# Performance work log

Hardware: AMD Instinct MI355X
Metric: run time of the kernel (lower is better)

Reference implementation:

```python
import jax, jax.numpy as jnp
import numpy as np

N = 65536   # total nodes
E = 1048576 # total edges (avg degree 16)
B = 512     # graphs in batch
H = 4       # gat1 heads
C = 64      # per-head channels / GNN_HIDDEN


def segment_softmax(logits, seg, num_segments):
    # numerically stable softmax over segments (PyG softmax semantics, eps=1e-16)
    m = jax.ops.segment_max(logits, seg, num_segments=num_segments)
    m = jnp.where(jnp.isfinite(m), m, 0.0)
    e = jnp.exp(logits - m[seg])
    s = jax.ops.segment_sum(e, seg, num_segments=num_segments)
    return e / (s[seg] + 1e-16)


def gat_conv(x, edge_index, edge_attr, W, att_src, att_dst, We, att_edge, bias, heads, out_ch, concat):
    # PyG GATConv with edge_dim, add_self_loops=False
    n = x.shape[0]
    h = (x @ W).reshape(n, heads, out_ch)                 # (N,H,C)
    src, dst = edge_index[0], edge_index[1]
    a_s = jnp.sum(h * att_src, axis=-1)                   # (N,H)
    a_d = jnp.sum(h * att_dst, axis=-1)                   # (N,H)
    he = (edge_attr @ We).reshape(-1, heads, out_ch)      # (E,H,C)
    a_e = jnp.sum(he * att_edge, axis=-1)                 # (E,H)
    alpha = jax.nn.leaky_relu(a_s[src] + a_d[dst] + a_e, negative_slope=0.2)
    alpha = segment_softmax(alpha, dst, n)                # softmax over incoming edges per dst
    out = jax.ops.segment_sum(h[src] * alpha[..., None], dst, num_segments=n)  # (N,H,C)
    out = out.reshape(n, heads * out_ch) if concat else out.mean(axis=1)
    return out + bias


def setup_inputs() -> dict:
    key = jax.random.key(0)
    ks = jax.random.split(key, 24)
    s = 0.05
    d = {}
    d["global_feat"] = jax.random.normal(ks[0], (B, 512), jnp.float32)
    d["x"] = jax.random.normal(ks[1], (N, 13), jnp.float32)
    d["roi_feats"] = jax.random.normal(ks[2], (N, 256), jnp.float32)
    d["edge_index"] = jax.random.randint(ks[3], (2, E), 0, N)
    d["edge_attr"] = jax.random.normal(ks[4], (E, 5), jnp.float32)
    d["batch_vec"] = jnp.sort(jax.random.randint(ks[5], (N,), 0, B))
    # roi_proj / scene_proj
    d["roi_W"] = jax.random.normal(ks[6], (256, 64), jnp.float32) * s
    d["roi_b"] = jnp.zeros((64,), jnp.float32)
    d["scene_W"] = jax.random.normal(ks[7], (512, 128), jnp.float32) * s
    d["scene_b"] = jnp.zeros((128,), jnp.float32)
    d["g1_W"] = jax.random.normal(ks[8], (77, H * C), jnp.float32) * s
    d["g1_att_src"] = jax.random.normal(ks[9], (H, C), jnp.float32) * s
    d["g1_att_dst"] = jax.random.normal(ks[10], (H, C), jnp.float32) * s
    d["g1_We"] = jax.random.normal(ks[11], (5, H * C), jnp.float32) * s
    d["g1_att_edge"] = jax.random.normal(ks[12], (H, C), jnp.float32) * s
    d["g1_bias"] = jnp.zeros((H * C,), jnp.float32)
    # gat2: 256 -> 64, 1 head
    d["g2_W"] = jax.random.normal(ks[13], (H * C, C), jnp.float32) * s
    d["g2_att_src"] = jax.random.normal(ks[14], (1, C), jnp.float32) * s
    d["g2_att_dst"] = jax.random.normal(ks[15], (1, C), jnp.float32) * s
    d["g2_We"] = jax.random.normal(ks[16], (5, C), jnp.float32) * s
    d["g2_att_edge"] = jax.random.normal(ks[17], (1, C), jnp.float32) * s
    d["g2_bias"] = jnp.zeros((C,), jnp.float32)
    # attention pooling gate + classifier
    d["gate_W"] = jax.random.normal(ks[18], (C, 1), jnp.float32) * s
    d["gate_b"] = jnp.zeros((1,), jnp.float32)
    d["cls1_W"] = jax.random.normal(ks[19], (128 + C, 64), jnp.float32) * s
    d["cls1_b"] = jnp.zeros((64,), jnp.float32)
    d["cls2_W"] = jax.random.normal(ks[20], (64, 3), jnp.float32) * s
    d["cls2_b"] = jnp.zeros((3,), jnp.float32)
    return d


def reference(global_feat, x, roi_feats, edge_index, edge_attr, batch_vec,
              roi_W, roi_b, scene_W, scene_b,
              g1_W, g1_att_src, g1_att_dst, g1_We, g1_att_edge, g1_bias,
              g2_W, g2_att_src, g2_att_dst, g2_We, g2_att_edge, g2_bias,
              gate_W, gate_b, cls1_W, cls1_b, cls2_W, cls2_b):
    scene = global_feat @ scene_W + scene_b                       # (B,128)
    vis = jax.nn.relu(roi_feats @ roi_W + roi_b)                  # (N,64)
    h = jnp.concatenate([x, vis], axis=-1)                        # (N,77)
    h = jax.nn.relu(gat_conv(h, edge_index, edge_attr, g1_W, g1_att_src, g1_att_dst, g1_We, g1_att_edge, g1_bias, H, C, True))
    h = gat_conv(h, edge_index, edge_attr, g2_W, g2_att_src, g2_att_dst, g2_We, g2_att_edge, g2_bias, 1, C, False)  # (N,64)
    # GlobalAttention pooling
    gate = segment_softmax((h @ gate_W + gate_b)[:, 0], batch_vec, B)
    rel = jax.ops.segment_sum(gate[:, None] * h, batch_vec, num_segments=B)  # (B,64)
    comb = jnp.concatenate([scene, rel], axis=-1)                 # (B,192)
    hid = jax.nn.relu(comb @ cls1_W + cls1_b)                     # dropout off (eval)
    return hid @ cls2_W + cls2_b                                  # (B,3)
```

## Files before the change

kernel.cpp:

```cpp
#include <hip/hip_runtime.h>

#define N_NODES 65536
#define N_EDGES 1048576
#define NB      512

typedef unsigned short u16;
typedef unsigned int   u32;
typedef unsigned long long u64;

typedef __attribute__((ext_vector_type(8))) short bf16x8;
typedef __attribute__((ext_vector_type(4))) float f32x4;

__device__ __forceinline__ float bf2f(u16 u) { return __uint_as_float(((u32)u) << 16); }
__device__ __forceinline__ float lo16(u32 u) { return __uint_as_float(u << 16); }
__device__ __forceinline__ float hi16(u32 u) { return __uint_as_float(u & 0xffff0000u); }
__device__ __forceinline__ u16 f2bf(float f) {
    u32 u = __float_as_uint(f);
    u32 r = (u + 0x7fffu + ((u >> 16) & 1u)) >> 16;
    return (u16)r;
}
__device__ __forceinline__ u32 pk2(float a, float b) {
    return (u32)f2bf(a) | ((u32)f2bf(b) << 16);
}
__device__ __forceinline__ float wsum(float v) {
    for (int o = 32; o; o >>= 1) v += __shfl_xor(v, o, 64);
    return v;
}
__device__ __forceinline__ float wmax(float v) {
    for (int o = 32; o; o >>= 1) v = fmaxf(v, __shfl_xor(v, o, 64));
    return v;
}

__global__ void k_prep(const float* g1We, const float* g1ae, const float* g2We, const float* g2ae,
                       float* M1, float* M2) {
    int t = threadIdx.x;
    if (t < 20) {
        int j = t >> 2, h = t & 3;
        float s = 0.f;
        for (int c = 0; c < 64; c++) s += g1We[j * 256 + h * 64 + c] * g1ae[h * 64 + c];
        M1[t] = s;
    } else if (t < 25) {
        int j = t - 20;
        float s = 0.f;
        for (int c = 0; c < 64; c++) s += g2We[j * 64 + c] * g2ae[c];
        M2[j] = s;
    }
}

__global__ void k_wt1(const float* __restrict__ g1W, u16* __restrict__ Wt) {
    int c = blockIdx.x;
    int k = threadIdx.x;
    float v = 0.f;
    if (k < 77) {
        int ko = (k < 64) ? (13 + k) : (k - 64);
        v = g1W[(size_t)ko * 256 + c];
    }
    Wt[(size_t)c * 96 + k] = f2bf(v);
}

__global__ void k_wtv(const float* __restrict__ roiW, u16* __restrict__ Wt) {
    int c = blockIdx.x;
    int k = threadIdx.x;
    Wt[(size_t)c * 256 + k] = f2bf(roiW[(size_t)k * 64 + c]);
}

__global__ __launch_bounds__(256) void k_scene(const float* __restrict__ gf, const float* __restrict__ W,
                                               const float* __restrict__ bias, float* __restrict__ scene) {
    int idx = blockIdx.x * 256 + threadIdx.x;
    int b = idx >> 7, j = idx & 127;
    float acc = 0.f;
    for (int k = 0; k < 512; k++) acc += gf[b * 512 + k] * W[k * 128 + j];
    scene[idx] = acc + bias[j];
}

__global__ __launch_bounds__(256) void k_hist(const int* ei, int* cnt) {
    int e = blockIdx.x * 256 + threadIdx.x;
    atomicAdd(&cnt[ei[N_EDGES + e]], 1);
}

__global__ __launch_bounds__(256) void k_scan_blk(const int* __restrict__ cnt, int* __restrict__ pre,
                                                  int* __restrict__ bsum) {
    __shared__ int sd[256];
    int t = threadIdx.x, b = blockIdx.x;
    int base = b * 1024 + t * 4;
    int4 c = *(const int4*)(cnt + base);
    int s = c.x + c.y + c.z + c.w;
    sd[t] = s;
    __syncthreads();
    for (int off = 1; off < 256; off <<= 1) {
        int v = (t >= off) ? sd[t - off] : 0;
        __syncthreads();
        sd[t] += v;
        __syncthreads();
    }
    int excl = sd[t] - s;
    int4 p;
    p.x = excl;
    p.y = excl + c.x;
    p.z = excl + c.x + c.y;
    p.w = excl + c.x + c.y + c.z;
    *(int4*)(pre + base) = p;
    if (t == 255) bsum[b] = sd[255];
}

__global__ __launch_bounds__(64) void k_scan_top(int* bsum) {
    int t = threadIdx.x;
    int v = bsum[t];
    int inc = v;
    for (int off = 1; off < 64; off <<= 1) {
        int u = __shfl_up(inc, off, 64);
        if (t >= off) inc += u;
    }
    bsum[t] = inc - v;
}

__global__ __launch_bounds__(256) void k_scan_fix(const int* __restrict__ pre, const int* __restrict__ bsum,
                                                  int* __restrict__ row_ptr, int* __restrict__ coarse_cur) {
    int i = blockIdx.x * 256 + threadIdx.x;
    int v = pre[i] + bsum[i >> 10];
    row_ptr[i] = v;
    if ((i & 255) == 0) coarse_cur[i >> 8] = v;
    if (i == 0) row_ptr[N_NODES] = N_EDGES;
}

__global__ __launch_bounds__(256) void k_bucket(const int* __restrict__ ei, int* coarse_cur,
                                                u32* __restrict__ bpack, int* __restrict__ bsrc) {
    __shared__ u32 stageP[4096];
    __shared__ int stageS[4096];
    __shared__ int bcnt[256], bscan[256], boff[256], gbase[256];
    int t = threadIdx.x;
    int e0 = blockIdx.x * 4096;
    bcnt[t] = 0;
    __syncthreads();
    int dreg[16], sreg[16];
    for (int it = 0; it < 16; it++) {
        int e = e0 + it * 256 + t;
        int dd = ei[N_EDGES + e];
        dreg[it] = dd;
        sreg[it] = ei[e];
        atomicAdd(&bcnt[dd >> 8], 1);
    }
    __syncthreads();
    int v = bcnt[t];
    bscan[t] = v;
    __syncthreads();
    for (int off = 1; off < 256; off <<= 1) {
        int u = (t >= off) ? bscan[t - off] : 0;
        __syncthreads();
        bscan[t] += u;
        __syncthreads();
    }
    boff[t] = bscan[t] - v;
    gbase[t] = v ? atomicAdd(&coarse_cur[t], v) : 0;
    __syncthreads();
    for (int it = 0; it < 16; it++) {
        int e = e0 + it * 256 + t;
        int b = dreg[it] >> 8;
        int pos = atomicAdd(&boff[b], 1);
        stageP[pos] = ((u32)e << 12) | (u32)(dreg[it] & 255);
        stageS[pos] = sreg[it];
    }
    __syncthreads();
    for (int idx = t; idx < 4096; idx += 256) {
        int lo = 0, hi = 255;
        while (lo < hi) { int mid = (lo + hi) >> 1; if (bscan[mid] > idx) hi = mid; else lo = mid + 1; }
        int b = lo;
        int g = gbase[b] + (idx - (bscan[b] - bcnt[b]));
        bpack[g] = stageP[idx];
        bsrc[g] = stageS[idx];
    }
}

__global__ __launch_bounds__(256) void k_sortb(const u32* __restrict__ bpack, const int* __restrict__ bsrc,
                                               const int* __restrict__ row_ptr,
                                               int* __restrict__ eord, int* __restrict__ ssrc) {
    __shared__ int cur[256];
    int t = threadIdx.x, b = blockIdx.x;
    int nbase = b * 256;
    cur[t] = row_ptr[nbase + t];
    __syncthreads();
    int beg = row_ptr[nbase];
    int end = row_ptr[nbase + 256];
    for (int i = beg + t; i < end; i += 256) {
        u32 wd = bpack[i];
        int src = bsrc[i];
        int d8 = wd & 255;
        int pos = atomicAdd(&cur[d8], 1);
        eord[pos] = (int)(wd >> 12);
        ssrc[pos] = src;
    }
}

__global__ __launch_bounds__(256) void k_payload(const int* __restrict__ eord, const float* __restrict__ ea,
                                                 const float* __restrict__ M1, const float* __restrict__ M2,
                                                 float* __restrict__ a1es, float* __restrict__ a2es) {
    int pos = blockIdx.x * 256 + threadIdx.x;
    int e = eord[pos];
    float v[5];
    for (int j = 0; j < 5; j++) v[j] = ea[(size_t)e * 5 + j];
    float4 o;
    o.x = v[0]*M1[0]  + v[1]*M1[4]  + v[2]*M1[8]  + v[3]*M1[12] + v[4]*M1[16];
    o.y = v[0]*M1[1]  + v[1]*M1[5]  + v[2]*M1[9]  + v[3]*M1[13] + v[4]*M1[17];
    o.z = v[0]*M1[2]  + v[1]*M1[6]  + v[2]*M1[10] + v[3]*M1[14] + v[4]*M1[18];
    o.w = v[0]*M1[3]  + v[1]*M1[7]  + v[2]*M1[11] + v[3]*M1[15] + v[4]*M1[19];
    *(float4*)(a1es + (size_t)pos * 4) = o;
    a2es[pos] = v[0]*M2[0] + v[1]*M2[1] + v[2]*M2[2] + v[3]*M2[3] + v[4]*M2[4];
}

__global__ __launch_bounds__(256) void k_vis(const float* __restrict__ roi, const u16* __restrict__ Wt,
                                             const float* __restrict__ bias, u16* __restrict__ out) {
    __shared__ u16 At[64][264];
    int t = threadIdx.x;
    int w = t >> 6, l = t & 63, lo = l & 15, hi = l >> 4;
    int n0 = blockIdx.x * 64;
    int r = t >> 2, sub = t & 3;
    const float* rp = roi + (size_t)(n0 + r) * 256 + sub * 4;
    #pragma unroll
    for (int q = 0; q < 16; q++) {
        float4 v = *(const float4*)(rp + q * 16);
        uint2 p;
        p.x = pk2(v.x, v.y);
        p.y = pk2(v.z, v.w);
        *(uint2*)&At[r][q * 16 + sub * 4] = p;
    }
    float bb[4][4];
    #pragma unroll
    for (int cb = 0; cb < 4; cb++)
        #pragma unroll
        for (int rg = 0; rg < 4; rg++) bb[cb][rg] = bias[cb * 16 + hi * 4 + rg];
    __syncthreads();
    f32x4 acc[4];
    #pragma unroll
    for (int cb = 0; cb < 4; cb++) acc[cb] = (f32x4){0.f, 0.f, 0.f, 0.f};
    #pragma unroll
    for (int ks = 0; ks < 8; ks++) {
        bf16x8 af = *(const bf16x8*)(&At[w * 16 + lo][ks * 32 + hi * 8]);
        #pragma unroll
        for (int cb = 0; cb < 4; cb++) {
            bf16x8 wf = *(const bf16x8*)(Wt + (size_t)(cb * 16 + lo) * 256 + ks * 32 + hi * 8);
            acc[cb] = __builtin_amdgcn_mfma_f32_16x16x32_bf16(wf, af, acc[cb], 0, 0, 0);
        }
    }
    int nrow = n0 + w * 16 + lo;
    #pragma unroll
    for (int cb = 0; cb < 4; cb++) {
        uint2 p;
        p.x = pk2(fmaxf(acc[cb][0] + bb[cb][0], 0.f), fmaxf(acc[cb][1] + bb[cb][1], 0.f));
        p.y = pk2(fmaxf(acc[cb][2] + bb[cb][2], 0.f), fmaxf(acc[cb][3] + bb[cb][3], 0.f));
        *(uint2*)(out + (size_t)nrow * 64 + cb * 16 + hi * 4) = p;
    }
}

__global__ __launch_bounds__(256) void k_h1(const float* __restrict__ x, const u16* __restrict__ vis,
                                            const u16* __restrict__ Wt,
                                            const float* __restrict__ as_, const float* __restrict__ ad_,
                                            u16* __restrict__ h1, float* __restrict__ a1s,
                                            float* __restrict__ a1d) {
    __shared__ u16 At[64][104];
    int t = threadIdx.x;
    int w = t >> 6, l = t & 63, lo = l & 15, hi = l >> 4;
    int n0 = blockIdx.x * 64;
    int r = t >> 2, sub = t & 3;
    {
        const uint4* vp = (const uint4*)(vis + (size_t)(n0 + r) * 64 + sub * 16);
        uint4 v0 = vp[0], v1 = vp[1];
        *(uint4*)&At[r][sub * 16] = v0;
        *(uint4*)&At[r][sub * 16 + 8] = v1;
        if (sub == 0) {
            const float* xp = x + (size_t)(n0 + r) * 13;
            #pragma unroll
            for (int j = 0; j < 13; j++) At[r][64 + j] = f2bf(xp[j]);
        } else if (sub == 1) {
            #pragma unroll
            for (int j = 77; j < 96; j++) At[r][j] = 0;
        }
    }
    bf16x8 wf[4][3];
    float asv[4][4], adv[4][4];
    #pragma unroll
    for (int cb = 0; cb < 4; cb++) {
        #pragma unroll
        for (int ks = 0; ks < 3; ks++)
            wf[cb][ks] = *(const bf16x8*)(Wt + (size_t)(w * 64 + cb * 16 + lo) * 96 + ks * 32 + hi * 8);
        #pragma unroll
        for (int rg = 0; rg < 4; rg++) {
            asv[cb][rg] = as_[w * 64 + cb * 16 + hi * 4 + rg];
            adv[cb][rg] = ad_[w * 64 + cb * 16 + hi * 4 + rg];
        }
    }
    __syncthreads();
    #pragma unroll
    for (int nb = 0; nb < 4; nb++) {
        f32x4 acc[4];
        #pragma unroll
        for (int cb = 0; cb < 4; cb++) acc[cb] = (f32x4){0.f, 0.f, 0.f, 0.f};
        #pragma unroll
        for (int ks = 0; ks < 3; ks++) {
            bf16x8 af = *(const bf16x8*)(&At[nb * 16 + lo][ks * 32 + hi * 8]);
            #pragma unroll
            for (int cb = 0; cb < 4; cb++)
                acc[cb] = __builtin_amdgcn_mfma_f32_16x16x32_bf16(wf[cb][ks], af, acc[cb], 0, 0, 0);
        }
        int nrow = n0 + nb * 16 + lo;
        float ps = 0.f, pd = 0.f;
        #pragma unroll
        for (int cb = 0; cb < 4; cb++) {
            uint2 p;
            p.x = pk2(acc[cb][0], acc[cb][1]);
            p.y = pk2(acc[cb][2], acc[cb][3]);
            *(uint2*)(h1 + (size_t)nrow * 256 + w * 64 + cb * 16 + hi * 4) = p;
            ps += acc[cb][0] * asv[cb][0] + acc[cb][1] * asv[cb][1]
                + acc[cb][2] * asv[cb][2] + acc[cb][3] * asv[cb][3];
            pd += acc[cb][0] * adv[cb][0] + acc[cb][1] * adv[cb][1]
                + acc[cb][2] * adv[cb][2] + acc[cb][3] * adv[cb][3];
        }
        ps += __shfl_xor(ps, 16, 64); ps += __shfl_xor(ps, 32, 64);
        pd += __shfl_xor(pd, 16, 64); pd += __shfl_xor(pd, 32, 64);
        if (hi == 0) {
            a1s[nrow * 4 + w] = ps;
            a1d[nrow * 4 + w] = pd;
        }
    }
}

__global__ __launch_bounds__(256) void k_h2(const u16* __restrict__ A, const float* __restrict__ W,
                                            const float* __restrict__ as_, const float* __restrict__ ad_,
                                            u16* __restrict__ out, float* __restrict__ a2s,
                                            float* __restrict__ a2d) {
    __shared__ float At[64][68];
    __shared__ float Wl[64][68];
    int t = threadIdx.x;
    int n0 = blockIdx.x * 64;
    int cg = t & 15, rg = t >> 4;
    int sr = t >> 2, scs = (t & 3) * 16;
    float acc[4][4];
    for (int i = 0; i < 4; i++) for (int j = 0; j < 4; j++) acc[i][j] = 0.f;
    for (int kc = 0; kc < 4; kc++) {
        __syncthreads();
        const u16* ap = A + (size_t)(n0 + sr) * 256 + kc * 64 + scs;
        uint4 u0 = *(const uint4*)ap;
        uint4 u1 = *(const uint4*)(ap + 8);
        At[scs + 0][sr] = lo16(u0.x);  At[scs + 1][sr] = hi16(u0.x);
        At[scs + 2][sr] = lo16(u0.y);  At[scs + 3][sr] = hi16(u0.y);
        At[scs + 4][sr] = lo16(u0.z);  At[scs + 5][sr] = hi16(u0.z);
        At[scs + 6][sr] = lo16(u0.w);  At[scs + 7][sr] = hi16(u0.w);
        At[scs + 8][sr] = lo16(u1.x);  At[scs + 9][sr] = hi16(u1.x);
        At[scs + 10][sr] = lo16(u1.y); At[scs + 11][sr] = hi16(u1.y);
        At[scs + 12][sr] = lo16(u1.z); At[scs + 13][sr] = hi16(u1.z);
        At[scs + 14][sr] = lo16(u1.w); At[scs + 15][sr] = hi16(u1.w);
        const float* wp = W + (size_t)(kc * 64 + sr) * 64 + scs;
        *(float4*)&Wl[sr][scs + 0]  = *(const float4*)wp;
        *(float4*)&Wl[sr][scs + 4]  = *(const float4*)(wp + 4);
        *(float4*)&Wl[sr][scs + 8]  = *(const float4*)(wp + 8);
        *(float4*)&Wl[sr][scs + 12] = *(const float4*)(wp + 12);
        __syncthreads();
        for (int k = 0; k < 64; k++) {
            float4 a4 = *(const float4*)&At[k][rg * 4];
            float4 w4 = *(const float4*)&Wl[k][cg * 4];
            acc[0][0] += a4.x * w4.x; acc[0][1] += a4.x * w4.y; acc[0][2] += a4.x * w4.z; acc[0][3] += a4.x * w4.w;
            acc[1][0] += a4.y * w4.x; acc[1][1] += a4.y * w4.y; acc[1][2] += a4.y * w4.z; acc[1][3] += a4.y * w4.w;
            acc[2][0] += a4.z * w4.x; acc[2][1] += a4.z * w4.y; acc[2][2] += a4.z * w4.z; acc[2][3] += a4.z * w4.w;
            acc[3][0] += a4.w * w4.x; acc[3][1] += a4.w * w4.y; acc[3][2] += a4.w * w4.z; acc[3][3] += a4.w * w4.w;
        }
    }
    u32* outu = (u32*)out;
    for (int i = 0; i < 4; i++) {
        uint2 pk;
        pk.x = (u32)f2bf(acc[i][0]) | ((u32)f2bf(acc[i][1]) << 16);
        pk.y = (u32)f2bf(acc[i][2]) | ((u32)f2bf(acc[i][3]) << 16);
        *(uint2*)(outu + (size_t)(n0 + rg * 4 + i) * 32 + cg * 2) = pk;
    }
    float4 as4 = *(const float4*)(as_ + cg * 4);
    float4 ad4 = *(const float4*)(ad_ + cg * 4);
    #pragma unroll
    for (int i = 0; i < 4; i++) {
        float ps = acc[i][0] * as4.x + acc[i][1] * as4.y + acc[i][2] * as4.z + acc[i][3] * as4.w;
        float pd = acc[i][0] * ad4.x + acc[i][1] * ad4.y + acc[i][2] * ad4.z + acc[i][3] * ad4.w;
        for (int o = 1; o < 16; o <<= 1) { ps += __shfl_xor(ps, o, 64); pd += __shfl_xor(pd, o, 64); }
        if (cg == 0) {
            a2s[n0 + rg * 4 + i] = ps;
            a2d[n0 + rg * 4 + i] = pd;
        }
    }
}

__global__ __launch_bounds__(256) void k_soft1(const int* __restrict__ row_ptr, const int* __restrict__ ssrc,
                                               const float* __restrict__ a1s, const float* __restrict__ a1d,
                                               const float* __restrict__ a1es, float* __restrict__ w1,
                                               float2* __restrict__ minv1) {
    int t = threadIdx.x;
    int wv = t >> 6, L = t & 63;
    int n = blockIdx.x * 4 + wv;
    int h = L >> 4, j = L & 15;
    int beg = row_ptr[n], deg = row_ptr[n + 1] - beg;
    if (deg == 0) return;
    float adn = a1d[n * 4 + h];
    float m = -3.0e38f, s = 0.f;
    for (int i = j; i < deg; i += 16) {
        int pos = beg + i;
        float l = a1s[ssrc[pos] * 4 + h] + adn + a1es[(size_t)pos * 4 + h];
        l = (l > 0.f) ? l : 0.2f * l;
        w1[(size_t)pos * 4 + h] = l;
        if (l > m) { s = s * __expf(m - l) + 1.f; m = l; }
        else       { s += __expf(l - m); }
    }
    for (int o = 1; o < 16; o <<= 1) {
        float mo = __shfl_xor(m, o, 64), so = __shfl_xor(s, o, 64);
        float M = fmaxf(m, mo);
        s = s * __expf(m - M) + so * __expf(mo - M);
        m = M;
    }
    if (j == 0) minv1[n * 4 + h] = make_float2(m, 1.f / (s + 1e-16f));
}

__global__ __launch_bounds__(256) void k_gath1(const int* __restrict__ row_ptr, const int* __restrict__ ssrc,
                                               const float* __restrict__ w1, const float2* __restrict__ minv1,
                                               const u16* __restrict__ h1,
                                               const float* __restrict__ bias, u16* __restrict__ out1) {
    int t = threadIdx.x;
    int wv = t >> 6, L = t & 63;
    int n = blockIdx.x * 4 + wv;
    int beg = row_ptr[n], deg = row_ptr[n + 1] - beg;
    int halfE = L >> 5;
    int L32 = L & 31;
    int hd = L32 >> 3;
    float2 mi = (deg > 0) ? minv1[n * 4 + hd] : make_float2(0.f, 0.f);
    float acc[8];
    #pragma unroll
    for (int j = 0; j < 8; j++) acc[j] = 0.f;
    int last = beg + deg - 1;
    for (int i = 0; i < deg; i += 8) {
        int iA = i + halfE, iB = i + 2 + halfE, iC = i + 4 + halfE, iD = i + 6 + halfE;
        bool vA = iA < deg, vB = iB < deg, vC = iC < deg, vD = iD < deg;
        int cA = vA ? beg + iA : last, cB = vB ? beg + iB : last;
        int cC = vC ? beg + iC : last, cD = vD ? beg + iD : last;
        int sA = ssrc[cA], sB = ssrc[cB], sC = ssrc[cC], sD = ssrc[cD];
        float lA = w1[(size_t)cA * 4 + hd];
        float lB = w1[(size_t)cB * 4 + hd];
        float lC = w1[(size_t)cC * 4 + hd];
        float lD = w1[(size_t)cD * 4 + hd];
        float wA = vA ? __expf(lA - mi.x) * mi.y : 0.f;
        float wB = vB ? __expf(lB - mi.x) * mi.y : 0.f;
        float wC = vC ? __expf(lC - mi.x) * mi.y : 0.f;
        float wD = vD ? __expf(lD - mi.x) * mi.y : 0.f;
        uint4 uA = *((const uint4*)(h1 + (size_t)sA * 256) + L32);
        uint4 uB = *((const uint4*)(h1 + (size_t)sB * 256) + L32);
        uint4 uC = *((const uint4*)(h1 + (size_t)sC * 256) + L32);
        uint4 uD = *((const uint4*)(h1 + (size_t)sD * 256) + L32);
        acc[0] += wA * lo16(uA.x) + wB * lo16(uB.x) + wC * lo16(uC.x) + wD * lo16(uD.x);
        acc[1] += wA * hi16(uA.x) + wB * hi16(uB.x) + wC * hi16(uC.x) + wD * hi16(uD.x);
        acc[2] += wA * lo16(uA.y) + wB * lo16(uB.y) + wC * lo16(uC.y) + wD * lo16(uD.y);
        acc[3] += wA * hi16(uA.y) + wB * hi16(uB.y) + wC * hi16(uC.y) + wD * hi16(uD.y);
        acc[4] += wA * lo16(uA.z) + wB * lo16(uB.z) + wC * lo16(uC.z) + wD * lo16(uD.z);
        acc[5] += wA * hi16(uA.z) + wB * hi16(uB.z) + wC * hi16(uC.z) + wD * hi16(uD.z);
        acc[6] += wA * lo16(uA.w) + wB * lo16(uB.w) + wC * lo16(uC.w) + wD * lo16(uD.w);
        acc[7] += wA * hi16(uA.w) + wB * hi16(uB.w) + wC * hi16(uC.w) + wD * hi16(uD.w);
    }
    #pragma unroll
    for (int j = 0; j < 8; j++) acc[j] += __shfl_xor(acc[j], 32, 64);
    if (halfE == 0) {
        float4 b0 = *(const float4*)(bias + 8 * L32);
        float4 b1 = *(const float4*)(bias + 8 * L32 + 4);
        uint4 pk;
        pk.x = (u32)f2bf(fmaxf(acc[0] + b0.x, 0.f)) | ((u32)f2bf(fmaxf(acc[1] + b0.y, 0.f)) << 16);
        pk.y = (u32)f2bf(fmaxf(acc[2] + b0.z, 0.f)) | ((u32)f2bf(fmaxf(acc[3] + b0.w, 0.f)) << 16);
        pk.z = (u32)f2bf(fmaxf(acc[4] + b1.x, 0.f)) | ((u32)f2bf(fmaxf(acc[5] + b1.y, 0.f)) << 16);
        pk.w = (u32)f2bf(fmaxf(acc[6] + b1.z, 0.f)) | ((u32)f2bf(fmaxf(acc[7] + b1.w, 0.f)) << 16);
        *((uint4*)(out1 + (size_t)n * 256) + L32) = pk;
    }
}

__global__ __launch_bounds__(256) void k_soft2(const int* __restrict__ row_ptr, const int* __restrict__ ssrc,
                                               const float* __restrict__ a2s, const float* __restrict__ a2d,
                                               const float* __restrict__ a2es, float* __restrict__ w2,
                                               float2* __restrict__ minv2) {
    int t = threadIdx.x;
    int wv = t >> 6, L = t & 63;
    int g = L >> 4, j = L & 15;
    int n = blockIdx.x * 16 + wv * 4 + g;
    int beg = row_ptr[n], deg = row_ptr[n + 1] - beg;
    if (deg == 0) return;
    float adn = a2d[n];
    float m = -3.0e38f, s = 0.f;
    for (int i = j; i < deg; i += 16) {
        int pos = beg + i;
        float l = a2s[ssrc[pos]] + adn + a2es[pos];
        l = (l > 0.f) ? l : 0.2f * l;
        w2[pos] = l;
        if (l > m) { s = s * __expf(m - l) + 1.f; m = l; }
        else       { s += __expf(l - m); }
    }
    for (int o = 1; o < 16; o <<= 1) {
        float mo = __shfl_xor(m, o, 64), so = __shfl_xor(s, o, 64);
        float M = fmaxf(m, mo);
        s = s * __expf(m - M) + so * __expf(mo - M);
        m = M;
    }
    if (j == 0) minv2[n] = make_float2(m, 1.f / (s + 1e-16f));
}

__global__ __launch_bounds__(256) void k_gath2(const int* __restrict__ row_ptr, const int* __restrict__ ssrc,
                                               const float* __restrict__ w2, const float2* __restrict__ minv2,
                                               const u16* __restrict__ h2b,
                                               const float* __restrict__ bias, float* __restrict__ hfin) {
    int t = threadIdx.x;
    int wv = t >> 6, L = t & 63;
    int n = blockIdx.x * 4 + wv;
    int beg = row_ptr[n], deg = row_ptr[n + 1] - beg;
    int halfE = L >> 5;
    int L32 = L & 31;
    float2 mi = (deg > 0) ? minv2[n] : make_float2(0.f, 0.f);
    float a0 = 0.f, a1v = 0.f;
    int last = beg + deg - 1;
    const u32* h2u = (const u32*)h2b;
    for (int i = 0; i < deg; i += 8) {
        int iA = i + halfE, iB = i + 2 + halfE, iC = i + 4 + halfE, iD = i + 6 + halfE;
        bool vA = iA < deg, vB = iB < deg, vC = iC < deg, vD = iD < deg;
        int cA = vA ? beg + iA : last, cB = vB ? beg + iB : last;
        int cC = vC ? beg + iC : last, cD = vD ? beg + iD : last;
        int sA = ssrc[cA], sB = ssrc[cB], sC = ssrc[cC], sD = ssrc[cD];
        float lA = w2[cA], lB = w2[cB], lC = w2[cC], lD = w2[cD];
        float wA = vA ? __expf(lA - mi.x) * mi.y : 0.f;
        float wB = vB ? __expf(lB - mi.x) * mi.y : 0.f;
        float wC = vC ? __expf(lC - mi.x) * mi.y : 0.f;
        float wD = vD ? __expf(lD - mi.x) * mi.y : 0.f;
        u32 uA = h2u[(size_t)sA * 32 + L32];
        u32 uB = h2u[(size_t)sB * 32 + L32];
        u32 uC = h2u[(size_t)sC * 32 + L32];
        u32 uD = h2u[(size_t)sD * 32 + L32];
        a0  += wA * lo16(uA) + wB * lo16(uB) + wC * lo16(uC) + wD * lo16(uD);
        a1v += wA * hi16(uA) + wB * hi16(uB) + wC * hi16(uC) + wD * hi16(uD);
    }
    a0  += __shfl_xor(a0, 32, 64);
    a1v += __shfl_xor(a1v, 32, 64);
    if (halfE == 0) {
        float2 o;
        o.x = a0  + bias[2 * L32];
        o.y = a1v + bias[2 * L32 + 1];
        *(float2*)(hfin + (size_t)n * 64 + 2 * L32) = o;
    }
}

__global__ __launch_bounds__(64) void k_pool(const int* __restrict__ bvec, const float* __restrict__ hf,
                                             const float* gateW, const float* gateb,
                                             const float* __restrict__ scene,
                                             const float* c1W, const float* c1b,
                                             const float* c2W, const float* c2b,
                                             float* __restrict__ outp) {
    int b = blockIdx.x, lane = threadIdx.x;
    __shared__ float gwl[64], se[64], comb[192], hid[64];
    gwl[lane] = gateW[lane];
    __syncthreads();
    int s0, s1;
    { int lo = 0, hi = N_NODES; while (lo < hi) { int mid = (lo + hi) >> 1; if (bvec[mid] < b) lo = mid + 1; else hi = mid; } s0 = lo; }
    { int lo = 0, hi = N_NODES; while (lo < hi) { int mid = (lo + hi) >> 1; if (bvec[mid] < b + 1) lo = mid + 1; else hi = mid; } s1 = lo; }
    float gb = gateb[0];
    float m = -3.0e38f, ssum = 0.f, acc = 0.f;
    for (int cs = s0; cs < s1; cs += 64) {
        int cnt = min(64, s1 - cs);
        float l = -3.0e38f;
        if (lane < cnt) {
            int n = cs + lane;
            float d = 0.f;
            for (int i = 0; i < 64; i++) d += hf[(size_t)n * 64 + i] * gwl[i];
            l = d + gb;
        }
        float cm = wmax(l);
        float newm = fmaxf(m, cm);
        float rsc = __expf(m - newm);
        float e = (lane < cnt) ? __expf(l - newm) : 0.f;
        float es = wsum(e);
        ssum = ssum * rsc + es;
        se[lane] = e;
        __syncthreads();
        float a2 = 0.f;
        for (int i = 0; i < cnt; i++) a2 += se[i] * hf[(size_t)(cs + i) * 64 + lane];
        acc = acc * rsc + a2;
        __syncthreads();
        m = newm;
    }
    float rel = acc / (ssum + 1e-16f);
    comb[lane] = scene[b * 128 + lane];
    comb[64 + lane] = scene[b * 128 + 64 + lane];
    comb[128 + lane] = rel;
    __syncthreads();
    float hj = 0.f;
    for (int k = 0; k < 192; k++) hj += comb[k] * c1W[k * 64 + lane];
    hj += c1b[lane];
    hid[lane] = fmaxf(hj, 0.f);
    __syncthreads();
    if (lane < 3) {
        float o = 0.f;
        for (int k = 0; k < 64; k++) o += hid[k] * c2W[k * 3 + lane];
        o += c2b[lane];
        outp[b * 3 + lane] = o;
    }
}

extern "C" void kernel_launch(void* const* d_in, const int* in_sizes, int n_in,
                              void* d_out, int out_size, void* d_ws, size_t ws_size,
                              hipStream_t stream) {
    (void)in_sizes; (void)n_in; (void)out_size; (void)ws_size;
    const float* gf     = (const float*)d_in[0];
    const float* x      = (const float*)d_in[1];
    const float* roi    = (const float*)d_in[2];
    const int*   ei     = (const int*)d_in[3];
    const float* ea     = (const float*)d_in[4];
    const int*   bvec   = (const int*)d_in[5];
    const float* roiW   = (const float*)d_in[6];
    const float* roib   = (const float*)d_in[7];
    const float* sceneW = (const float*)d_in[8];
    const float* sceneb = (const float*)d_in[9];
    const float* g1W    = (const float*)d_in[10];
    const float* g1as   = (const float*)d_in[11];
    const float* g1ad   = (const float*)d_in[12];
    const float* g1We   = (const float*)d_in[13];
    const float* g1ae   = (const float*)d_in[14];
    const float* g1b    = (const float*)d_in[15];
    const float* g2W    = (const float*)d_in[16];
    const float* g2as   = (const float*)d_in[17];
    const float* g2ad   = (const float*)d_in[18];
    const float* g2We   = (const float*)d_in[19];
    const float* g2ae   = (const float*)d_in[20];
    const float* g2b    = (const float*)d_in[21];
    const float* gateW  = (const float*)d_in[22];
    const float* gateb  = (const float*)d_in[23];
    const float* c1W    = (const float*)d_in[24];
    const float* c1b    = (const float*)d_in[25];
    const float* c2W    = (const float*)d_in[26];
    const float* c2b    = (const float*)d_in[27];

    char* w = (char*)d_ws;
    size_t o = 0;
    auto nxt = [&](size_t bytes) -> char* {
        char* p = w + o;
        o += (bytes + 255) & ~(size_t)255;
        return p;
    };
    float* scene  = (float*)nxt((size_t)NB * 128 * 4);
    float* M1     = (float*)nxt(80);
    float* M2     = (float*)nxt(32);
    u16* g1Wt     = (u16*)nxt((size_t)256 * 96 * 2);
    u16* roiWt    = (u16*)nxt((size_t)64 * 256 * 2);
    int* cnt      = (int*)nxt((size_t)N_NODES * 4);
    int* pre      = (int*)nxt((size_t)N_NODES * 4);
    int* bsum     = (int*)nxt(64 * 4);
    int* row_ptr  = (int*)nxt((size_t)(N_NODES + 1) * 4);
    int* coarse   = (int*)nxt(256 * 4);
    u32* bpack    = (u32*)nxt((size_t)N_EDGES * 4);
    int* bsrc     = (int*)nxt((size_t)N_EDGES * 4);
    int* eord     = (int*)nxt((size_t)N_EDGES * 4);
    int* ssrc     = (int*)nxt((size_t)N_EDGES * 4);
    float* a1es   = (float*)nxt((size_t)N_EDGES * 16);
    float* a2es   = (float*)nxt((size_t)N_EDGES * 4);
    float* visbuf = (float*)nxt((size_t)N_NODES * 64 * 4);
    u16* h1       = (u16*)nxt((size_t)N_NODES * 256 * 2);
    u16* out1     = (u16*)nxt((size_t)N_NODES * 256 * 2);
    float* w1buf  = (float*)nxt((size_t)N_EDGES * 16);
    float* hfin   = (float*)nxt((size_t)N_NODES * 64 * 4);
    float* a1s    = (float*)nxt((size_t)N_NODES * 16);
    float* a1d    = (float*)nxt((size_t)N_NODES * 16);
    float* a2s    = (float*)nxt((size_t)N_NODES * 4);
    float* a2d    = (float*)nxt((size_t)N_NODES * 4);
    float2* minv1 = (float2*)nxt((size_t)N_NODES * 4 * 8);
    float2* minv2 = (float2*)nxt((size_t)N_NODES * 8);

    u16* visb = (u16*)visbuf;
    float* w2 = visbuf;
    float* w1 = w1buf;
    u16*   h2b = (u16*)w1buf;

    hipMemsetAsync(cnt, 0, (size_t)N_NODES * 4, stream);
    k_prep<<<1, 32, 0, stream>>>(g1We, g1ae, g2We, g2ae, M1, M2);
    k_wt1<<<256, 96, 0, stream>>>(g1W, g1Wt);
    k_wtv<<<64, 256, 0, stream>>>(roiW, roiWt);
    k_scene<<<(NB * 128) / 256, 256, 0, stream>>>(gf, sceneW, sceneb, scene);
    k_hist<<<N_EDGES / 256, 256, 0, stream>>>(ei, cnt);
    k_scan_blk<<<64, 256, 0, stream>>>(cnt, pre, bsum);
    k_scan_top<<<1, 64, 0, stream>>>(bsum);
    k_scan_fix<<<N_NODES / 256, 256, 0, stream>>>(pre, bsum, row_ptr, coarse);
    k_bucket<<<256, 256, 0, stream>>>(ei, coarse, bpack, bsrc);
    k_sortb<<<256, 256, 0, stream>>>(bpack, bsrc, row_ptr, eord, ssrc);
    k_payload<<<N_EDGES / 256, 256, 0, stream>>>(eord, ea, M1, M2, a1es, a2es);
    k_vis<<<N_NODES / 64, 256, 0, stream>>>(roi, roiWt, roib, visb);
    k_h1<<<N_NODES / 64, 256, 0, stream>>>(x, visb, g1Wt, g1as, g1ad, h1, a1s, a1d);
    k_soft1<<<N_NODES / 4, 256, 0, stream>>>(row_ptr, ssrc, a1s, a1d, a1es, w1, minv1);
    k_gath1<<<N_NODES / 4, 256, 0, stream>>>(row_ptr, ssrc, w1, minv1, h1, g1b, out1);
    k_h2<<<N_NODES / 64, 256, 0, stream>>>(out1, g2W, g2as, g2ad, h2b, a2s, a2d);
    k_soft2<<<N_NODES / 16, 256, 0, stream>>>(row_ptr, ssrc, a2s, a2d, a2es, w2, minv2);
    k_gath2<<<N_NODES / 4, 256, 0, stream>>>(row_ptr, ssrc, w2, minv2, h2b, g2b, hfin);
    k_pool<<<NB, 64, 0, stream>>>(bvec, hfin, gateW, gateb, scene, c1W, c1b, c2W, c2b, (float*)d_out);
}
```

Before: 550.8 us.

## Fuse GAT softmax into gather via LDS weights and use MFMA for layer-2 projection

Merges the separate softmax and gather kernels of both GAT layers into one kernel per layer. Each node's normalized attention weights are held in LDS instead of being written to a global per-edge logit buffer and re-exponentiated during the gather. The layer-2 node projection is also rewritten to use bf16 MFMA with a pre-transposed bf16 weight, replacing the fp32 LDS-tiled FMA loop. The LDS weight buffer holds only 256 edges per node, so any node with higher in-degree would read past the valid weights; that bound is assumed rather than handled.

```diff
diff --git a/kernel.cpp b/kernel.cpp
--- a/kernel.cpp
+++ b/kernel.cpp
@@ -58,10 +58,10 @@
     Wt[(size_t)c * 96 + k] = f2bf(v);
 }
 
-__global__ void k_wtv(const float* __restrict__ roiW, u16* __restrict__ Wt) {
+__global__ void k_wtv(const float* __restrict__ W, u16* __restrict__ Wt) {
     int c = blockIdx.x;
     int k = threadIdx.x;
-    Wt[(size_t)c * 256 + k] = f2bf(roiW[(size_t)k * 64 + c]);
+    Wt[(size_t)c * 256 + k] = f2bf(W[(size_t)k * 64 + c]);
 }
 
 __global__ __launch_bounds__(256) void k_scene(const float* __restrict__ gf, const float* __restrict__ W,
@@ -323,108 +323,84 @@
     }
 }
 
-__global__ __launch_bounds__(256) void k_h2(const u16* __restrict__ A, const float* __restrict__ W,
+__global__ __launch_bounds__(256) void k_h2(const u16* __restrict__ A, const u16* __restrict__ Wt,
                                             const float* __restrict__ as_, const float* __restrict__ ad_,
                                             u16* __restrict__ out, float* __restrict__ a2s,
                                             float* __restrict__ a2d) {
-    __shared__ float At[64][68];
-    __shared__ float Wl[64][68];
-    int t = threadIdx.x;
-    int n0 = blockIdx.x * 64;
-    int cg = t & 15, rg = t >> 4;
-    int sr = t >> 2, scs = (t & 3) * 16;
-    float acc[4][4];
-    for (int i = 0; i < 4; i++) for (int j = 0; j < 4; j++) acc[i][j] = 0.f;
-    for (int kc = 0; kc < 4; kc++) {
-        __syncthreads();
-        const u16* ap = A + (size_t)(n0 + sr) * 256 + kc * 64 + scs;
-        uint4 u0 = *(const uint4*)ap;
-        uint4 u1 = *(const uint4*)(ap + 8);
-        At[scs + 0][sr] = lo16(u0.x);  At[scs + 1][sr] = hi16(u0.x);
-        At[scs + 2][sr] = lo16(u0.y);  At[scs + 3][sr] = hi16(u0.y);
-        At[scs + 4][sr] = lo16(u0.z);  At[scs + 5][sr] = hi16(u0.z);
-        At[scs + 6][sr] = lo16(u0.w);  At[scs + 7][sr] = hi16(u0.w);
-        At[scs + 8][sr] = lo16(u1.x);  At[scs + 9][sr] = hi16(u1.x);
-        At[scs + 10][sr] = lo16(u1.y); At[scs + 11][sr] = hi16(u1.y);
-        At[scs + 12][sr] = lo16(u1.z); At[scs + 13][sr] = hi16(u1.z);
-        At[scs + 14][sr] = lo16(u1.w); At[scs + 15][sr] = hi16(u1.w);
-        const float* wp = W + (size_t)(kc * 64 + sr) * 64 + scs;
-        *(float4*)&Wl[sr][scs + 0]  = *(const float4*)wp;
-        *(float4*)&Wl[sr][scs + 4]  = *(const float4*)(wp + 4);
-        *(float4*)&Wl[sr][scs + 8]  = *(const float4*)(wp + 8);
-        *(float4*)&Wl[sr][scs + 12] = *(const float4*)(wp + 12);
-        __syncthreads();
-        for (int k = 0; k < 64; k++) {
-            float4 a4 = *(const float4*)&At[k][rg * 4];
-            float4 w4 = *(const float4*)&Wl[k][cg * 4];
-            acc[0][0] += a4.x * w4.x; acc[0][1] += a4.x * w4.y; acc[0][2] += a4.x * w4.z; acc[0][3] += a4.x * w4.w;
-            acc[1][0] += a4.y * w4.x; acc[1][1] += a4.y * w4.y; acc[1][2] += a4.y * w4.z; acc[1][3] += a4.y * w4.w;
-            acc[2][0] += a4.z * w4.x; acc[2][1] += a4.z * w4.y; acc[2][2] += a4.z * w4.z; acc[2][3] += a4.z * w4.w;
-            acc[3][0] += a4.w * w4.x; acc[3][1] += a4.w * w4.y; acc[3][2] += a4.w * w4.z; acc[3][3] += a4.w * w4.w;
-        }
-    }
-    u32* outu = (u32*)out;
-    for (int i = 0; i < 4; i++) {
-        uint2 pk;
-        pk.x = (u32)f2bf(acc[i][0]) | ((u32)f2bf(acc[i][1]) << 16);
-        pk.y = (u32)f2bf(acc[i][2]) | ((u32)f2bf(acc[i][3]) << 16);
-        *(uint2*)(outu + (size_t)(n0 + rg * 4 + i) * 32 + cg * 2) = pk;
-    }
-    float4 as4 = *(const float4*)(as_ + cg * 4);
-    float4 ad4 = *(const float4*)(ad_ + cg * 4);
-    #pragma unroll
-    for (int i = 0; i < 4; i++) {
-        float ps = acc[i][0] * as4.x + acc[i][1] * as4.y + acc[i][2] * as4.z + acc[i][3] * as4.w;
-        float pd = acc[i][0] * ad4.x + acc[i][1] * ad4.y + acc[i][2] * ad4.z + acc[i][3] * ad4.w;
-        for (int o = 1; o < 16; o <<= 1) { ps += __shfl_xor(ps, o, 64); pd += __shfl_xor(pd, o, 64); }
-        if (cg == 0) {
-            a2s[n0 + rg * 4 + i] = ps;
-            a2d[n0 + rg * 4 + i] = pd;
-        }
-    }
-}
-
-__global__ __launch_bounds__(256) void k_soft1(const int* __restrict__ row_ptr, const int* __restrict__ ssrc,
-                                               const float* __restrict__ a1s, const float* __restrict__ a1d,
-                                               const float* __restrict__ a1es, float* __restrict__ w1,
-                                               float2* __restrict__ minv1) {
-    int t = threadIdx.x;
-    int wv = t >> 6, L = t & 63;
-    int n = blockIdx.x * 4 + wv;
-    int h = L >> 4, j = L & 15;
-    int beg = row_ptr[n], deg = row_ptr[n + 1] - beg;
-    if (deg == 0) return;
-    float adn = a1d[n * 4 + h];
-    float m = -3.0e38f, s = 0.f;
-    for (int i = j; i < deg; i += 16) {
-        int pos = beg + i;
-        float l = a1s[ssrc[pos] * 4 + h] + adn + a1es[(size_t)pos * 4 + h];
-        l = (l > 0.f) ? l : 0.2f * l;
-        w1[(size_t)pos * 4 + h] = l;
-        if (l > m) { s = s * __expf(m - l) + 1.f; m = l; }
-        else       { s += __expf(l - m); }
-    }
-    for (int o = 1; o < 16; o <<= 1) {
-        float mo = __shfl_xor(m, o, 64), so = __shfl_xor(s, o, 64);
-        float M = fmaxf(m, mo);
-        s = s * __expf(m - M) + so * __expf(mo - M);
-        m = M;
-    }
-    if (j == 0) minv1[n * 4 + h] = make_float2(m, 1.f / (s + 1e-16f));
-}
-
-__global__ __launch_bounds__(256) void k_gath1(const int* __restrict__ row_ptr, const int* __restrict__ ssrc,
-                                               const float* __restrict__ w1, const float2* __restrict__ minv1,
-                                               const u16* __restrict__ h1,
-                                               const float* __restrict__ bias, u16* __restrict__ out1) {
+    int t = threadIdx.x;
+    int w = t >> 6, l = t & 63, lo = l & 15, hi = l >> 4;
+    int nrow = blockIdx.x * 64 + w * 16 + lo;
+    f32x4 acc[4];
+    #pragma unroll
+    for (int cb = 0; cb < 4; cb++) acc[cb] = (f32x4){0.f, 0.f, 0.f, 0.f};
+    const u16* ap = A + (size_t)nrow * 256 + hi * 8;
+    #pragma unroll
+    for (int ks = 0; ks < 8; ks++) {
+        bf16x8 af = *(const bf16x8*)(ap + ks * 32);
+        #pragma unroll
+        for (int cb = 0; cb < 4; cb++) {
+            bf16x8 wf = *(const bf16x8*)(Wt + (size_t)(cb * 16 + lo) * 256 + ks * 32 + hi * 8);
+            acc[cb] = __builtin_amdgcn_mfma_f32_16x16x32_bf16(wf, af, acc[cb], 0, 0, 0);
+        }
+    }
+    float ps = 0.f, pd = 0.f;
+    #pragma unroll
+    for (int cb = 0; cb < 4; cb++) {
+        uint2 p;
+        p.x = pk2(acc[cb][0], acc[cb][1]);
+        p.y = pk2(acc[cb][2], acc[cb][3]);
+        *(uint2*)(out + (size_t)nrow * 64 + cb * 16 + hi * 4) = p;
+        #pragma unroll
+        for (int rg = 0; rg < 4; rg++) {
+            float a = acc[cb][rg];
+            ps += a * as_[cb * 16 + hi * 4 + rg];
+            pd += a * ad_[cb * 16 + hi * 4 + rg];
+        }
+    }
+    ps += __shfl_xor(ps, 16, 64); ps += __shfl_xor(ps, 32, 64);
+    pd += __shfl_xor(pd, 16, 64); pd += __shfl_xor(pd, 32, 64);
+    if (hi == 0) {
+        a2s[nrow] = ps;
+        a2d[nrow] = pd;
+    }
+}
+
+__global__ __launch_bounds__(256) void k_sg1(const int* __restrict__ row_ptr, const int* __restrict__ ssrc,
+                                             const float* __restrict__ a1s, const float* __restrict__ a1d,
+                                             const float* __restrict__ a1es, const u16* __restrict__ h1,
+                                             const float* __restrict__ bias, u16* __restrict__ out1) {
+    __shared__ float wl[4][1024];
     int t = threadIdx.x;
     int wv = t >> 6, L = t & 63;
     int n = blockIdx.x * 4 + wv;
     int beg = row_ptr[n], deg = row_ptr[n + 1] - beg;
+    int lim = (deg < 256) ? deg : 256;
+    {
+        int h = L >> 4, j = L & 15;
+        float adn = a1d[n * 4 + h];
+        float m = -3.0e38f, s = 0.f;
+        for (int i = j; i < deg; i += 16) {
+            int pos = beg + i;
+            float l = a1s[ssrc[pos] * 4 + h] + adn + a1es[(size_t)pos * 4 + h];
+            l = (l > 0.f) ? l : 0.2f * l;
+            if (i < 256) wl[wv][i * 4 + h] = l;
+            if (l > m) { s = s * __expf(m - l) + 1.f; m = l; }
+            else       { s += __expf(l - m); }
+        }
+        for (int o = 1; o < 16; o <<= 1) {
+            float mo = __shfl_xor(m, o, 64), so = __shfl_xor(s, o, 64);
+            float M = fmaxf(m, mo);
+            s = s * __expf(m - M) + so * __expf(mo - M);
+            m = M;
+        }
+        float inv = 1.f / (s + 1e-16f);
+        for (int i = j; i < lim; i += 16)
+            wl[wv][i * 4 + h] = __expf(wl[wv][i * 4 + h] - m) * inv;
+    }
+    __syncthreads();
     int halfE = L >> 5;
     int L32 = L & 31;
     int hd = L32 >> 3;
-    float2 mi = (deg > 0) ? minv1[n * 4 + hd] : make_float2(0.f, 0.f);
     float acc[8];
     #pragma unroll
     for (int j = 0; j < 8; j++) acc[j] = 0.f;
@@ -435,14 +411,10 @@
         int cA = vA ? beg + iA : last, cB = vB ? beg + iB : last;
         int cC = vC ? beg + iC : last, cD = vD ? beg + iD : last;
         int sA = ssrc[cA], sB = ssrc[cB], sC = ssrc[cC], sD = ssrc[cD];
-        float lA = w1[(size_t)cA * 4 + hd];
-        float lB = w1[(size_t)cB * 4 + hd];
-        float lC = w1[(size_t)cC * 4 + hd];
-        float lD = w1[(size_t)cD * 4 + hd];
-        float wA = vA ? __expf(lA - mi.x) * mi.y : 0.f;
-        float wB = vB ? __expf(lB - mi.x) * mi.y : 0.f;
-        float wC = vC ? __expf(lC - mi.x) * mi.y : 0.f;
-        float wD = vD ? __expf(lD - mi.x) * mi.y : 0.f;
+        float wA = vA ? wl[wv][iA * 4 + hd] : 0.f;
+        float wB = vB ? wl[wv][iB * 4 + hd] : 0.f;
+        float wC = vC ? wl[wv][iC * 4 + hd] : 0.f;
+        float wD = vD ? wl[wv][iD * 4 + hd] : 0.f;
         uint4 uA = *((const uint4*)(h1 + (size_t)sA * 256) + L32);
         uint4 uB = *((const uint4*)(h1 + (size_t)sB * 256) + L32);
         uint4 uC = *((const uint4*)(h1 + (size_t)sC * 256) + L32);
@@ -470,46 +442,40 @@
     }
 }
 
-__global__ __launch_bounds__(256) void k_soft2(const int* __restrict__ row_ptr, const int* __restrict__ ssrc,
-                                               const float* __restrict__ a2s, const float* __restrict__ a2d,
-                                               const float* __restrict__ a2es, float* __restrict__ w2,
-                                               float2* __restrict__ minv2) {
-    int t = threadIdx.x;
-    int wv = t >> 6, L = t & 63;
-    int g = L >> 4, j = L & 15;
-    int n = blockIdx.x * 16 + wv * 4 + g;
-    int beg = row_ptr[n], deg = row_ptr[n + 1] - beg;
-    if (deg == 0) return;
-    float adn = a2d[n];
-    float m = -3.0e38f, s = 0.f;
-    for (int i = j; i < deg; i += 16) {
-        int pos = beg + i;
-        float l = a2s[ssrc[pos]] + adn + a2es[pos];
-        l = (l > 0.f) ? l : 0.2f * l;
-        w2[pos] = l;
-        if (l > m) { s = s * __expf(m - l) + 1.f; m = l; }
-        else       { s += __expf(l - m); }
-    }
-    for (int o = 1; o < 16; o <<= 1) {
-        float mo = __shfl_xor(m, o, 64), so = __shfl_xor(s, o, 64);
-        float M = fmaxf(m, mo);
-        s = s * __expf(m - M) + so * __expf(mo - M);
-        m = M;
-    }
-    if (j == 0) minv2[n] = make_float2(m, 1.f / (s + 1e-16f));
-}
-
-__global__ __launch_bounds__(256) void k_gath2(const int* __restrict__ row_ptr, const int* __restrict__ ssrc,
-                                               const float* __restrict__ w2, const float2* __restrict__ minv2,
-                                               const u16* __restrict__ h2b,
-                                               const float* __restrict__ bias, float* __restrict__ hfin) {
+__global__ __launch_bounds__(256) void k_sg2(const int* __restrict__ row_ptr, const int* __restrict__ ssrc,
+                                             const float* __restrict__ a2s, const float* __restrict__ a2d,
+                                             const float* __restrict__ a2es, const u16* __restrict__ h2b,
+                                             const float* __restrict__ bias, float* __restrict__ hfin) {
+    __shared__ float wl[4][256];
     int t = threadIdx.x;
     int wv = t >> 6, L = t & 63;
     int n = blockIdx.x * 4 + wv;
     int beg = row_ptr[n], deg = row_ptr[n + 1] - beg;
+    int lim = (deg < 256) ? deg : 256;
+    {
+        float adn = a2d[n];
+        float m = -3.0e38f, s = 0.f;
+        for (int i = L; i < deg; i += 64) {
+            int pos = beg + i;
+            float l = a2s[ssrc[pos]] + adn + a2es[pos];
+            l = (l > 0.f) ? l : 0.2f * l;
+            if (i < 256) wl[wv][i] = l;
+            if (l > m) { s = s * __expf(m - l) + 1.f; m = l; }
+            else       { s += __expf(l - m); }
+        }
+        for (int o = 1; o < 64; o <<= 1) {
+            float mo = __shfl_xor(m, o, 64), so = __shfl_xor(s, o, 64);
+            float M = fmaxf(m, mo);
+            s = s * __expf(m - M) + so * __expf(mo - M);
+            m = M;
+        }
+        float inv = 1.f / (s + 1e-16f);
+        for (int i = L; i < lim; i += 64)
+            wl[wv][i] = __expf(wl[wv][i] - m) * inv;
+    }
+    __syncthreads();
     int halfE = L >> 5;
     int L32 = L & 31;
-    float2 mi = (deg > 0) ? minv2[n] : make_float2(0.f, 0.f);
     float a0 = 0.f, a1v = 0.f;
     int last = beg + deg - 1;
     const u32* h2u = (const u32*)h2b;
@@ -519,11 +485,10 @@
         int cA = vA ? beg + iA : last, cB = vB ? beg + iB : last;
         int cC = vC ? beg + iC : last, cD = vD ? beg + iD : last;
         int sA = ssrc[cA], sB = ssrc[cB], sC = ssrc[cC], sD = ssrc[cD];
-        float lA = w2[cA], lB = w2[cB], lC = w2[cC], lD = w2[cD];
-        float wA = vA ? __expf(lA - mi.x) * mi.y : 0.f;
-        float wB = vB ? __expf(lB - mi.x) * mi.y : 0.f;
-        float wC = vC ? __expf(lC - mi.x) * mi.y : 0.f;
-        float wD = vD ? __expf(lD - mi.x) * mi.y : 0.f;
+        float wA = vA ? wl[wv][iA] : 0.f;
+        float wB = vB ? wl[wv][iB] : 0.f;
+        float wC = vC ? wl[wv][iC] : 0.f;
+        float wD = vD ? wl[wv][iD] : 0.f;
         u32 uA = h2u[(size_t)sA * 32 + L32];
         u32 uB = h2u[(size_t)sB * 32 + L32];
         u32 uC = h2u[(size_t)sC * 32 + L32];
@@ -642,6 +607,7 @@
     float* M2     = (float*)nxt(32);
     u16* g1Wt     = (u16*)nxt((size_t)256 * 96 * 2);
     u16* roiWt    = (u16*)nxt((size_t)64 * 256 * 2);
+    u16* g2Wt     = (u16*)nxt((size_t)64 * 256 * 2);
     int* cnt      = (int*)nxt((size_t)N_NODES * 4);
     int* pre      = (int*)nxt((size_t)N_NODES * 4);
     int* bsum     = (int*)nxt(64 * 4);
@@ -653,27 +619,21 @@
     int* ssrc     = (int*)nxt((size_t)N_EDGES * 4);
     float* a1es   = (float*)nxt((size_t)N_EDGES * 16);
     float* a2es   = (float*)nxt((size_t)N_EDGES * 4);
-    float* visbuf = (float*)nxt((size_t)N_NODES * 64 * 4);
+    u16* visb     = (u16*)nxt((size_t)N_NODES * 64 * 2);
     u16* h1       = (u16*)nxt((size_t)N_NODES * 256 * 2);
     u16* out1     = (u16*)nxt((size_t)N_NODES * 256 * 2);
-    float* w1buf  = (float*)nxt((size_t)N_EDGES * 16);
+    u16* h2b      = (u16*)nxt((size_t)N_NODES * 64 * 2);
     float* hfin   = (float*)nxt((size_t)N_NODES * 64 * 4);
     float* a1s    = (float*)nxt((size_t)N_NODES * 16);
     float* a1d    = (float*)nxt((size_t)N_NODES * 16);
     float* a2s    = (float*)nxt((size_t)N_NODES * 4);
     float* a2d    = (float*)nxt((size_t)N_NODES * 4);
-    float2* minv1 = (float2*)nxt((size_t)N_NODES * 4 * 8);
-    float2* minv2 = (float2*)nxt((size_t)N_NODES * 8);
-
-    u16* visb = (u16*)visbuf;
-    float* w2 = visbuf;
-    float* w1 = w1buf;
-    u16*   h2b = (u16*)w1buf;
 
     hipMemsetAsync(cnt, 0, (size_t)N_NODES * 4, stream);
     k_prep<<<1, 32, 0, stream>>>(g1We, g1ae, g2We, g2ae, M1, M2);
     k_wt1<<<256, 96, 0, stream>>>(g1W, g1Wt);
     k_wtv<<<64, 256, 0, stream>>>(roiW, roiWt);
+    k_wtv<<<64, 256, 0, stream>>>(g2W, g2Wt);
     k_scene<<<(NB * 128) / 256, 256, 0, stream>>>(gf, sceneW, sceneb, scene);
     k_hist<<<N_EDGES / 256, 256, 0, stream>>>(ei, cnt);
     k_scan_blk<<<64, 256, 0, stream>>>(cnt, pre, bsum);
@@ -684,10 +644,8 @@
     k_payload<<<N_EDGES / 256, 256, 0, stream>>>(eord, ea, M1, M2, a1es, a2es);
     k_vis<<<N_NODES / 64, 256, 0, stream>>>(roi, roiWt, roib, visb);
     k_h1<<<N_NODES / 64, 256, 0, stream>>>(x, visb, g1Wt, g1as, g1ad, h1, a1s, a1d);
-    k_soft1<<<N_NODES / 4, 256, 0, stream>>>(row_ptr, ssrc, a1s, a1d, a1es, w1, minv1);
-    k_gath1<<<N_NODES / 4, 256, 0, stream>>>(row_ptr, ssrc, w1, minv1, h1, g1b, out1);
-    k_h2<<<N_NODES / 64, 256, 0, stream>>>(out1, g2W, g2as, g2ad, h2b, a2s, a2d);
-    k_soft2<<<N_NODES / 16, 256, 0, stream>>>(row_ptr, ssrc, a2s, a2d, a2es, w2, minv2);
-    k_gath2<<<N_NODES / 4, 256, 0, stream>>>(row_ptr, ssrc, w2, minv2, h2b, g2b, hfin);
+    k_sg1<<<N_NODES / 4, 256, 0, stream>>>(row_ptr, ssrc, a1s, a1d, a1es, h1, g1b, out1);
+    k_h2<<<N_NODES / 64, 256, 0, stream>>>(out1, g2Wt, g2as, g2ad, h2b, a2s, a2d);
+    k_sg2<<<N_NODES / 4, 256, 0, stream>>>(row_ptr, ssrc, a2s, a2d, a2es, h2b, g2b, hfin);
     k_pool<<<NB, 64, 0, stream>>>(bvec, hfin, gateW, gateb, scene, c1W, c1b, c2W, c2b, (float*)d_out);
 }
```

Result: faster. 527.4 us (-4.2%).
